# Kernel tuning notes

Measured on AMD Instinct MI355X. Metric: run time of the kernel, lower is better.

## Reference

```python
import jax, jax.numpy as jnp
import numpy as np

NUM_HEADS = 1
SR = 8
DIM = 64
EPS = 1e-5


def _layernorm(x, g, b):
    mu = jnp.mean(x, axis=-1, keepdims=True)
    var = jnp.mean(jnp.square(x - mu), axis=-1, keepdims=True)
    return (x - mu) * jax.lax.rsqrt(var + EPS) * g + b


def _sr_pool(x, h, w, s):
    # x: [B, N, C] with N = h*w -> avg-pool spatially by s -> [B, (h//s)*(w//s), C]
    B, N, C = x.shape
    xi = x.transpose(0, 2, 1).reshape(B, C, h, w)
    xi = xi.reshape(B, C, h // s, s, w // s, s).mean(axis=(3, 5))
    return xi.reshape(B, C, -1).transpose(0, 2, 1)


def _branch(q, x_src, h, w, kv_w, norm_g, norm_b, proj_w, proj_b, scale):
    B, N, C = x_src.shape
    hd = C // NUM_HEADS
    xp = _layernorm(_sr_pool(x_src, h, w, SR), norm_g, norm_b)  # [B, Nk, C]
    kv = (xp @ kv_w.T).reshape(B, -1, 2, NUM_HEADS, hd).transpose(2, 0, 3, 1, 4)
    k, v = kv[0], kv[1]  # [B, H, Nk, hd]
    attn = jnp.einsum('bhnd,bhmd->bhnm', q, k) * scale  # [B, H, N, Nk]
    attn = jax.nn.softmax(attn, axis=-1)
    out = jnp.einsum('bhnm,bhmd->bhnd', attn, v)
    out = out.transpose(0, 2, 1, 3).reshape(B, N, C)
    return out @ proj_w.T + proj_b


def setup_inputs() -> dict:
    key = jax.random.key(0)
    ks = jax.random.split(key, 10)
    B, h, w, C = 4, 128, 128, DIM
    N = h * w
    sd = 1.0 / np.sqrt(C)
    return {
        'x1': jax.random.normal(ks[0], (B, N, C), jnp.float32),
        'x2': jax.random.normal(ks[1], (B, N, C), jnp.float32),
        'h': h,
        'w': w,
        'q1_w': jax.random.uniform(ks[2], (C, C), jnp.float32, -sd, sd),
        'kv1_w': jax.random.uniform(ks[3], (2 * C, C), jnp.float32, -sd, sd),
        'kv2_w': jax.random.uniform(ks[4], (2 * C, C), jnp.float32, -sd, sd),
        'norm1_g': jnp.ones((C,), jnp.float32),
        'norm1_b': jnp.zeros((C,), jnp.float32),
        'norm2_g': jnp.ones((C,), jnp.float32),
        'norm2_b': jnp.zeros((C,), jnp.float32),
        'proj1_w': jax.random.uniform(ks[5], (C, C), jnp.float32, -sd, sd),
        'proj1_b': jnp.zeros((C,), jnp.float32),
        'proj2_w': jax.random.uniform(ks[6], (C, C), jnp.float32, -sd, sd),
        'proj2_b': jnp.zeros((C,), jnp.float32),
    }


def reference(x1, x2, h, w, q1_w, kv1_w, kv2_w, norm1_g, norm1_b,
              norm2_g, norm2_b, proj1_w, proj1_b, proj2_w, proj2_b):
    B, N, C = x1.shape
    hd = C // NUM_HEADS
    scale = hd ** -0.5
    # NOTE: original code uses self.q1 for BOTH q1 and q2 (bug-faithful).
    q1 = (x1 @ q1_w.T).reshape(B, N, NUM_HEADS, hd).transpose(0, 2, 1, 3)
    q2 = (x2 @ q1_w.T).reshape(B, N, NUM_HEADS, hd).transpose(0, 2, 1, 3)
    o1 = _branch(q1, x1, h, w, kv1_w, norm1_g, norm1_b, proj1_w, proj1_b, scale)
    o2 = _branch(q2, x2, h, w, kv2_w, norm2_g, norm2_b, proj2_w, proj2_b, scale)
    return (o1, o2)
```

## Files before the change

### kernel.cpp

```cpp
#include <hip/hip_runtime.h>
#include <math.h>

#define CH 64
#define SRV 8
#define HV 128
#define WV 128
#define NTOK (HV*WV)
#define NKV 256
#define POOLW 16
#define KVIMG 65536

typedef __attribute__((ext_vector_type(8))) short bf16x8;
typedef __attribute__((ext_vector_type(16))) float f32x16;

__device__ __forceinline__ unsigned short f2bf(float x) {
    unsigned u = __float_as_uint(x);
    return (unsigned short)((u + 0x7fffu + ((u >> 16) & 1u)) >> 16);
}
__device__ __forceinline__ unsigned pkbf(float a, float b) {
    return (unsigned)f2bf(a) | ((unsigned)f2bf(b) << 16);
}
__device__ __forceinline__ void swap32(unsigned a, unsigned b, unsigned &oa, unsigned &ob) {
    unsigned ax = (unsigned)__shfl_xor((int)a, 32);
    unsigned bx = (unsigned)__shfl_xor((int)b, 32);
    const bool lo = (threadIdx.x & 32) == 0;
    oa = lo ? a : bx;
    ob = lo ? ax : b;
}

__global__ __launch_bounds__(64) void fused_pool_ln_kv(
    const float* __restrict__ x1, const float* __restrict__ x2,
    const float* __restrict__ kv1w, const float* __restrict__ kv2w,
    const float* __restrict__ n1g, const float* __restrict__ n1b,
    const float* __restrict__ n2g, const float* __restrict__ n2b,
    const float* __restrict__ q1w,
    const float* __restrict__ p1w, const float* __restrict__ p2w,
    char* __restrict__ kvbuf, int B)
{
    const int c = threadIdx.x;
    const int blk = blockIdx.x;
    const int m = blk % NKV;
    const int t = blk / NKV;
    const int b = t % B;
    const int branch = t / B;

    const float* x   = branch ? x2   : x1;
    const float* kvw = branch ? kv2w : kv1w;
    const float* g   = branch ? n2g  : n1g;
    const float* be  = branch ? n2b  : n1b;
    const float* pw  = branch ? p2w  : p1w;

    const int ph = m / POOLW, pwc = m % POOLW;
    const float* xb = x + ((size_t)b * NTOK) * CH;

    float sum = 0.f;
    for (int dy = 0; dy < SRV; ++dy) {
        const int y = ph * SRV + dy;
        const float* xr = xb + ((size_t)(y * WV + pwc * SRV)) * CH + c;
        #pragma unroll
        for (int dx = 0; dx < SRV; ++dx)
            sum += xr[dx * CH];
    }
    float v = sum * (1.f / 64.f);

    float mu = v;
    #pragma unroll
    for (int o = 32; o; o >>= 1) mu += __shfl_xor(mu, o);
    mu *= (1.f / 64.f);
    float d = v - mu;
    float var = d * d;
    #pragma unroll
    for (int o = 32; o; o >>= 1) var += __shfl_xor(var, o);
    var *= (1.f / 64.f);
    float xp = d * rsqrtf(var + 1e-5f) * g[c] + be[c];

    __shared__ float sx[CH];
    __shared__ float kb[CH];
    __shared__ float vb[CH];
    sx[c] = xp;
    __syncthreads();

    float ka = 0.f, va = 0.f;
    #pragma unroll
    for (int dd = 0; dd < CH; ++dd) {
        const float xd = sx[dd];
        ka += xd * kvw[(size_t)c * CH + dd];
        va += xd * kvw[(size_t)(CH + c) * CH + dd];
    }
    kb[c] = ka;
    vb[c] = va;
    __syncthreads();

    float k2 = 0.f, v2 = 0.f;
    #pragma unroll
    for (int j = 0; j < CH; ++j) {
        k2 += kb[j] * q1w[(size_t)j * CH + c];
        v2 += vb[j] * pw[(size_t)c * CH + j];
    }
    k2 *= 0.125f;

    char* base = kvbuf + (size_t)(branch * B + b) * KVIMG;
    *(unsigned short*)(base + m * 128 + ((2 * c) ^ ((m & 7) << 4))) = f2bf(k2);
    *(unsigned short*)(base + 32768 + c * 512 + ((2 * m) ^ ((c & 7) << 4))) = f2bf(v2);
}

__global__ __launch_bounds__(256, 2) void fused_attn_mfma(
    const float* __restrict__ x1, const float* __restrict__ x2,
    const char* __restrict__ kvbuf,
    const float* __restrict__ p1b, const float* __restrict__ p2b,
    float* __restrict__ out, int B)
{
    extern __shared__ char KV[];
    const int tiles = NTOK / 128;
    const int blk = blockIdx.x;
    const int branch = blk / (B * tiles);
    const int rem = blk - branch * (B * tiles);
    const int b = rem / tiles;
    const int tile = rem - b * tiles;
    const int rowbase = tile * 128;

    const float* x  = branch ? x2  : x1;
    const float* pb = branch ? p2b : p1b;
    const char* kvbase = kvbuf + (size_t)(branch * B + b) * KVIMG;

    {
        const int4* src = (const int4*)kvbase;
        int4* dst = (int4*)KV;
        #pragma unroll
        for (int i = 0; i < 16; ++i)
            dst[i * 256 + threadIdx.x] = src[i * 256 + threadIdx.x];
    }
    __syncthreads();

    const int tid = threadIdx.x;
    const int lane = tid & 63;
    const int wv = tid >> 6;
    const int l31 = lane & 31;
    const int hi = lane >> 5;
    const int hi16 = hi * 16, hi8 = hi * 8;
    const int row = rowbase + wv * 32 + l31;
    const float* xr = x + ((size_t)b * NTOK + row) * CH;

    union U8 { bf16x8 v; unsigned d[4]; };

    bf16x8 xf[4];
    #pragma unroll
    for (int kc = 0; kc < 4; ++kc) {
        const float* xp = xr + kc * 16 + hi8;
        const float4 a  = *(const float4*)xp;
        const float4 c4 = *(const float4*)(xp + 4);
        U8 u;
        u.d[0] = pkbf(a.x, a.y);  u.d[1] = pkbf(a.z, a.w);
        u.d[2] = pkbf(c4.x, c4.y); u.d[3] = pkbf(c4.z, c4.w);
        xf[kc] = u.v;
    }

    f32x16 acc[8];
    #pragma unroll
    for (int kb8 = 0; kb8 < 8; ++kb8)
        #pragma unroll
        for (int r = 0; r < 16; ++r) acc[kb8][r] = 0.f;

    #pragma unroll
    for (int kc = 0; kc < 4; ++kc) {
        #pragma unroll
        for (int kb8 = 0; kb8 < 8; ++kb8) {
            const int key = kb8 * 32 + l31;
            const int off = key * 128 + ((kc * 32 + hi16) ^ ((key & 7) << 4));
            const bf16x8 kf = *(const bf16x8*)(KV + off);
            acc[kb8] = __builtin_amdgcn_mfma_f32_32x32x16_bf16(kf, xf[kc], acc[kb8], 0, 0, 0);
        }
    }

    float lsum = 0.f;
    bf16x8 pvB[16];
    #pragma unroll
    for (int kb8 = 0; kb8 < 8; ++kb8) {
        float p[16];
        #pragma unroll
        for (int r = 0; r < 16; ++r) { p[r] = __expf(acc[kb8][r]); lsum += p[r]; }
        unsigned q0, q1, q2, q3;
        U8 u;
        swap32(pkbf(p[0], p[1]),  pkbf(p[4], p[5]),  q0, q2);
        swap32(pkbf(p[2], p[3]),  pkbf(p[6], p[7]),  q1, q3);
        u.d[0] = q0; u.d[1] = q1; u.d[2] = q2; u.d[3] = q3;
        pvB[2 * kb8] = u.v;
        swap32(pkbf(p[8], p[9]),   pkbf(p[12], p[13]), q0, q2);
        swap32(pkbf(p[10], p[11]), pkbf(p[14], p[15]), q1, q3);
        u.d[0] = q0; u.d[1] = q1; u.d[2] = q2; u.d[3] = q3;
        pvB[2 * kb8 + 1] = u.v;
    }
    const float lfull = lsum + __shfl_xor(lsum, 32);
    const float invl = 1.f / lfull;

    f32x16 oac[2];
    #pragma unroll
    for (int df = 0; df < 2; ++df)
        #pragma unroll
        for (int r = 0; r < 16; ++r) oac[df][r] = 0.f;

    #pragma unroll
    for (int t = 0; t < 16; ++t) {
        #pragma unroll
        for (int df = 0; df < 2; ++df) {
            const int d = df * 32 + l31;
            const int off = 32768 + d * 512 + ((t * 32 + hi16) ^ ((d & 7) << 4));
            const bf16x8 vf = *(const bf16x8*)(KV + off);
            oac[df] = __builtin_amdgcn_mfma_f32_32x32x16_bf16(vf, pvB[t], oac[df], 0, 0, 0);
        }
    }

    float* orow = out + ((size_t)(branch * B + b) * NTOK + row) * CH;
    #pragma unroll
    for (int df = 0; df < 2; ++df) {
        #pragma unroll
        for (int q = 0; q < 4; ++q) {
            const int d0 = df * 32 + q * 8 + hi * 4;
            const float4 bias = *(const float4*)(pb + d0);
            float4 w;
            w.x = oac[df][4 * q + 0] * invl + bias.x;
            w.y = oac[df][4 * q + 1] * invl + bias.y;
            w.z = oac[df][4 * q + 2] * invl + bias.z;
            w.w = oac[df][4 * q + 3] * invl + bias.w;
            *(float4*)(orow + d0) = w;
        }
    }
}

extern "C" void kernel_launch(void* const* d_in, const int* in_sizes, int n_in,
                              void* d_out, int out_size, void* d_ws, size_t ws_size,
                              hipStream_t stream) {
    const float* x1   = (const float*)d_in[0];
    const float* x2   = (const float*)d_in[1];
    const float* q1w  = (const float*)d_in[4];
    const float* kv1w = (const float*)d_in[5];
    const float* kv2w = (const float*)d_in[6];
    const float* n1g  = (const float*)d_in[7];
    const float* n1b  = (const float*)d_in[8];
    const float* n2g  = (const float*)d_in[9];
    const float* n2b  = (const float*)d_in[10];
    const float* p1w  = (const float*)d_in[11];
    const float* p1b  = (const float*)d_in[12];
    const float* p2w  = (const float*)d_in[13];
    const float* p2b  = (const float*)d_in[14];

    const int B = in_sizes[0] / (NTOK * CH);
    char* kvbuf = (char*)d_ws;

    fused_pool_ln_kv<<<2 * B * NKV, 64, 0, stream>>>(
        x1, x2, kv1w, kv2w, n1g, n1b, n2g, n2b, q1w, p1w, p2w, kvbuf, B);

    fused_attn_mfma<<<2 * B * (NTOK / 128), 256, KVIMG, stream>>>(
        x1, x2, kvbuf, p1b, p2b, (float*)d_out, B);
}
```

Measured before the change: 46.23 us.

## Process two row tiles per block with async KV LDS loads and prefetch

```diff
diff --git a/kernel.cpp b/kernel.cpp
--- a/kernel.cpp
+++ b/kernel.cpp
@@ -9,6 +9,7 @@
 #define NKV 256
 #define POOLW 16
 #define KVIMG 65536
+#define NITER 2
 
 typedef __attribute__((ext_vector_type(8))) short bf16x8;
 typedef __attribute__((ext_vector_type(16))) float f32x16;
@@ -17,18 +18,34 @@
     unsigned u = __float_as_uint(x);
     return (unsigned short)((u + 0x7fffu + ((u >> 16) & 1u)) >> 16);
 }
-__device__ __forceinline__ unsigned pkbf(float a, float b) {
-    return (unsigned)f2bf(a) | ((unsigned)f2bf(b) << 16);
-}
-__device__ __forceinline__ void swap32(unsigned a, unsigned b, unsigned &oa, unsigned &ob) {
+
+__device__ __forceinline__ unsigned cvt_pk(float lo, float hi) {
+    unsigned r;
+    asm("v_cvt_pk_bf16_f32 %0, %1, %2" : "=v"(r) : "v"(lo), "v"(hi));
+    return r;
+}
+
+__device__ __forceinline__ void plswap(unsigned a, unsigned b,
+                                       unsigned &oa, unsigned &ob) {
+#if __has_builtin(__builtin_amdgcn_permlane32_swap)
+    auto r = __builtin_amdgcn_permlane32_swap(a, b, false, false);
+    oa = r[0]; ob = r[1];
+#else
     unsigned ax = (unsigned)__shfl_xor((int)a, 32);
     unsigned bx = (unsigned)__shfl_xor((int)b, 32);
     const bool lo = (threadIdx.x & 32) == 0;
     oa = lo ? a : bx;
     ob = lo ? ax : b;
-}
-
-__global__ __launch_bounds__(64) void fused_pool_ln_kv(
+#endif
+}
+
+__device__ __forceinline__ void gload_lds16(const void* g, void* l) {
+    __builtin_amdgcn_global_load_lds(
+        (const __attribute__((address_space(1))) void*)g,
+        (__attribute__((address_space(3))) void*)l, 16, 0, 0);
+}
+
+__global__ __launch_bounds__(256) void fused_pool_ln_kv(
     const float* __restrict__ x1, const float* __restrict__ x2,
     const float* __restrict__ kv1w, const float* __restrict__ kv2w,
     const float* __restrict__ n1g, const float* __restrict__ n1b,
@@ -37,16 +54,17 @@
     const float* __restrict__ p1w, const float* __restrict__ p2w,
     char* __restrict__ kvbuf, int B)
 {
-    const int c = threadIdx.x;
-    const int blk = blockIdx.x;
-    const int m = blk % NKV;
-    const int t = blk / NKV;
+    const int c  = threadIdx.x & 63;
+    const int wv = threadIdx.x >> 6;
+    const int g  = blockIdx.x * 4 + wv;
+    const int m = g % NKV;
+    const int t = g / NKV;
     const int b = t % B;
     const int branch = t / B;
 
     const float* x   = branch ? x2   : x1;
     const float* kvw = branch ? kv2w : kv1w;
-    const float* g   = branch ? n2g  : n1g;
+    const float* gg  = branch ? n2g  : n1g;
     const float* be  = branch ? n2b  : n1b;
     const float* pw  = branch ? p2w  : p1w;
 
@@ -72,30 +90,30 @@
     #pragma unroll
     for (int o = 32; o; o >>= 1) var += __shfl_xor(var, o);
     var *= (1.f / 64.f);
-    float xp = d * rsqrtf(var + 1e-5f) * g[c] + be[c];
-
-    __shared__ float sx[CH];
-    __shared__ float kb[CH];
-    __shared__ float vb[CH];
-    sx[c] = xp;
+    float xp = d * rsqrtf(var + 1e-5f) * gg[c] + be[c];
+
+    __shared__ float sx[4][CH];
+    __shared__ float kb[4][CH];
+    __shared__ float vb[4][CH];
+    sx[wv][c] = xp;
     __syncthreads();
 
     float ka = 0.f, va = 0.f;
     #pragma unroll
     for (int dd = 0; dd < CH; ++dd) {
-        const float xd = sx[dd];
+        const float xd = sx[wv][dd];
         ka += xd * kvw[(size_t)c * CH + dd];
         va += xd * kvw[(size_t)(CH + c) * CH + dd];
     }
-    kb[c] = ka;
-    vb[c] = va;
+    kb[wv][c] = ka;
+    vb[wv][c] = va;
     __syncthreads();
 
     float k2 = 0.f, v2 = 0.f;
     #pragma unroll
     for (int j = 0; j < CH; ++j) {
-        k2 += kb[j] * q1w[(size_t)j * CH + c];
-        v2 += vb[j] * pw[(size_t)c * CH + j];
+        k2 += kb[wv][j] * q1w[(size_t)j * CH + c];
+        v2 += vb[wv][j] * pw[(size_t)c * CH + j];
     }
     k2 *= 0.125f;
 
@@ -111,26 +129,16 @@
     float* __restrict__ out, int B)
 {
     extern __shared__ char KV[];
-    const int tiles = NTOK / 128;
+    const int tpg = NTOK / (128 * NITER);
     const int blk = blockIdx.x;
-    const int branch = blk / (B * tiles);
-    const int rem = blk - branch * (B * tiles);
-    const int b = rem / tiles;
-    const int tile = rem - b * tiles;
-    const int rowbase = tile * 128;
+    const int branch = blk / (B * tpg);
+    const int rem = blk - branch * (B * tpg);
+    const int b = rem / tpg;
+    const int tg = rem - b * tpg;
 
     const float* x  = branch ? x2  : x1;
     const float* pb = branch ? p2b : p1b;
     const char* kvbase = kvbuf + (size_t)(branch * B + b) * KVIMG;
-
-    {
-        const int4* src = (const int4*)kvbase;
-        int4* dst = (int4*)KV;
-        #pragma unroll
-        for (int i = 0; i < 16; ++i)
-            dst[i * 256 + threadIdx.x] = src[i * 256 + threadIdx.x];
-    }
-    __syncthreads();
 
     const int tid = threadIdx.x;
     const int lane = tid & 63;
@@ -138,91 +146,126 @@
     const int l31 = lane & 31;
     const int hi = lane >> 5;
     const int hi16 = hi * 16, hi8 = hi * 8;
-    const int row = rowbase + wv * 32 + l31;
-    const float* xr = x + ((size_t)b * NTOK + row) * CH;
+    const int swz = (l31 & 7) << 4;
+
+    {
+        #pragma unroll
+        for (int i = 0; i < 16; ++i)
+            gload_lds16(kvbase + i * 4096 + wv * 1024 + (lane << 4),
+                        KV + i * 4096 + wv * 1024);
+    }
+
+    const int rowb0 = tg * (128 * NITER) + wv * 32 + l31;
+    float4 xq[8];
+    {
+        const float* xr = x + ((size_t)b * NTOK + rowb0) * CH;
+        #pragma unroll
+        for (int kc = 0; kc < 4; ++kc) {
+            xq[2 * kc]     = *(const float4*)(xr + kc * 16 + hi8);
+            xq[2 * kc + 1] = *(const float4*)(xr + kc * 16 + hi8 + 4);
+        }
+    }
+    __syncthreads();
 
     union U8 { bf16x8 v; unsigned d[4]; };
 
-    bf16x8 xf[4];
-    #pragma unroll
-    for (int kc = 0; kc < 4; ++kc) {
-        const float* xp = xr + kc * 16 + hi8;
-        const float4 a  = *(const float4*)xp;
-        const float4 c4 = *(const float4*)(xp + 4);
-        U8 u;
-        u.d[0] = pkbf(a.x, a.y);  u.d[1] = pkbf(a.z, a.w);
-        u.d[2] = pkbf(c4.x, c4.y); u.d[3] = pkbf(c4.z, c4.w);
-        xf[kc] = u.v;
-    }
-
-    f32x16 acc[8];
-    #pragma unroll
-    for (int kb8 = 0; kb8 < 8; ++kb8)
-        #pragma unroll
-        for (int r = 0; r < 16; ++r) acc[kb8][r] = 0.f;
-
-    #pragma unroll
-    for (int kc = 0; kc < 4; ++kc) {
-        #pragma unroll
-        for (int kb8 = 0; kb8 < 8; ++kb8) {
-            const int key = kb8 * 32 + l31;
-            const int off = key * 128 + ((kc * 32 + hi16) ^ ((key & 7) << 4));
-            const bf16x8 kf = *(const bf16x8*)(KV + off);
-            acc[kb8] = __builtin_amdgcn_mfma_f32_32x32x16_bf16(kf, xf[kc], acc[kb8], 0, 0, 0);
-        }
-    }
-
-    float lsum = 0.f;
-    bf16x8 pvB[16];
-    #pragma unroll
-    for (int kb8 = 0; kb8 < 8; ++kb8) {
-        float p[16];
-        #pragma unroll
-        for (int r = 0; r < 16; ++r) { p[r] = __expf(acc[kb8][r]); lsum += p[r]; }
-        unsigned q0, q1, q2, q3;
-        U8 u;
-        swap32(pkbf(p[0], p[1]),  pkbf(p[4], p[5]),  q0, q2);
-        swap32(pkbf(p[2], p[3]),  pkbf(p[6], p[7]),  q1, q3);
-        u.d[0] = q0; u.d[1] = q1; u.d[2] = q2; u.d[3] = q3;
-        pvB[2 * kb8] = u.v;
-        swap32(pkbf(p[8], p[9]),   pkbf(p[12], p[13]), q0, q2);
-        swap32(pkbf(p[10], p[11]), pkbf(p[14], p[15]), q1, q3);
-        u.d[0] = q0; u.d[1] = q1; u.d[2] = q2; u.d[3] = q3;
-        pvB[2 * kb8 + 1] = u.v;
-    }
-    const float lfull = lsum + __shfl_xor(lsum, 32);
-    const float invl = 1.f / lfull;
-
-    f32x16 oac[2];
-    #pragma unroll
-    for (int df = 0; df < 2; ++df)
-        #pragma unroll
-        for (int r = 0; r < 16; ++r) oac[df][r] = 0.f;
-
-    #pragma unroll
-    for (int t = 0; t < 16; ++t) {
+    #pragma unroll
+    for (int it = 0; it < NITER; ++it) {
+        const int row = rowb0 + it * 128;
+
+        bf16x8 xf[4];
+        #pragma unroll
+        for (int kc = 0; kc < 4; ++kc) {
+            const float4 a  = xq[2 * kc];
+            const float4 c4 = xq[2 * kc + 1];
+            U8 u;
+            u.d[0] = cvt_pk(a.x, a.y);   u.d[1] = cvt_pk(a.z, a.w);
+            u.d[2] = cvt_pk(c4.x, c4.y); u.d[3] = cvt_pk(c4.z, c4.w);
+            xf[kc] = u.v;
+        }
+        if (it + 1 < NITER) {
+            const float* xr = x + ((size_t)b * NTOK + row + 128) * CH;
+            #pragma unroll
+            for (int kc = 0; kc < 4; ++kc) {
+                xq[2 * kc]     = *(const float4*)(xr + kc * 16 + hi8);
+                xq[2 * kc + 1] = *(const float4*)(xr + kc * 16 + hi8 + 4);
+            }
+        }
+
+        float lsum0 = 0.f, lsum1 = 0.f;
+        bf16x8 pvB[16];
+        #pragma unroll
+        for (int kp = 0; kp < 4; ++kp) {
+            f32x16 a0, a1;
+            #pragma unroll
+            for (int r = 0; r < 16; ++r) { a0[r] = 0.f; a1[r] = 0.f; }
+            const int key0 = kp * 64 + l31;
+            __builtin_amdgcn_s_setprio(1);
+            #pragma unroll
+            for (int kc = 0; kc < 4; ++kc) {
+                const int co = (kc * 32 + hi16) ^ swz;
+                const bf16x8 k0 = *(const bf16x8*)(KV + key0 * 128 + co);
+                const bf16x8 k1 = *(const bf16x8*)(KV + (key0 + 32) * 128 + co);
+                a0 = __builtin_amdgcn_mfma_f32_32x32x16_bf16(k0, xf[kc], a0, 0, 0, 0);
+                a1 = __builtin_amdgcn_mfma_f32_32x32x16_bf16(k1, xf[kc], a1, 0, 0, 0);
+            }
+            __builtin_amdgcn_s_setprio(0);
+            float p0[16], p1[16];
+            #pragma unroll
+            for (int r = 0; r < 16; ++r) {
+                p0[r] = __expf(a0[r]); lsum0 += p0[r];
+                p1[r] = __expf(a1[r]); lsum1 += p1[r];
+            }
+            #pragma unroll
+            for (int h = 0; h < 2; ++h) {
+                const float* p = h ? p1 : p0;
+                unsigned q0, q1, q2, q3;
+                U8 u;
+                plswap(cvt_pk(p[0], p[1]), cvt_pk(p[4], p[5]), q0, q2);
+                plswap(cvt_pk(p[2], p[3]), cvt_pk(p[6], p[7]), q1, q3);
+                u.d[0] = q0; u.d[1] = q1; u.d[2] = q2; u.d[3] = q3;
+                pvB[4 * kp + 2 * h] = u.v;
+                plswap(cvt_pk(p[8], p[9]),   cvt_pk(p[12], p[13]), q0, q2);
+                plswap(cvt_pk(p[10], p[11]), cvt_pk(p[14], p[15]), q1, q3);
+                u.d[0] = q0; u.d[1] = q1; u.d[2] = q2; u.d[3] = q3;
+                pvB[4 * kp + 2 * h + 1] = u.v;
+            }
+        }
+        float lsum = lsum0 + lsum1;
+        const float lfull = lsum + __shfl_xor(lsum, 32);
+        const float invl = 1.f / lfull;
+
+        f32x16 oac[2];
+        #pragma unroll
+        for (int df = 0; df < 2; ++df)
+            #pragma unroll
+            for (int r = 0; r < 16; ++r) oac[df][r] = 0.f;
+
+        __builtin_amdgcn_s_setprio(1);
+        #pragma unroll
+        for (int t = 0; t < 16; ++t) {
+            const int co = (t * 32 + hi16) ^ swz;
+            const bf16x8 vf0 = *(const bf16x8*)(KV + 32768 + l31 * 512 + co);
+            const bf16x8 vf1 = *(const bf16x8*)(KV + 32768 + (32 + l31) * 512 + co);
+            oac[0] = __builtin_amdgcn_mfma_f32_32x32x16_bf16(vf0, pvB[t], oac[0], 0, 0, 0);
+            oac[1] = __builtin_amdgcn_mfma_f32_32x32x16_bf16(vf1, pvB[t], oac[1], 0, 0, 0);
+        }
+        __builtin_amdgcn_s_setprio(0);
+
+        float* orow = out + ((size_t)(branch * B + b) * NTOK + row) * CH;
         #pragma unroll
         for (int df = 0; df < 2; ++df) {
-            const int d = df * 32 + l31;
-            const int off = 32768 + d * 512 + ((t * 32 + hi16) ^ ((d & 7) << 4));
-            const bf16x8 vf = *(const bf16x8*)(KV + off);
-            oac[df] = __builtin_amdgcn_mfma_f32_32x32x16_bf16(vf, pvB[t], oac[df], 0, 0, 0);
-        }
-    }
-
-    float* orow = out + ((size_t)(branch * B + b) * NTOK + row) * CH;
-    #pragma unroll
-    for (int df = 0; df < 2; ++df) {
-        #pragma unroll
-        for (int q = 0; q < 4; ++q) {
-            const int d0 = df * 32 + q * 8 + hi * 4;
-            const float4 bias = *(const float4*)(pb + d0);
-            float4 w;
-            w.x = oac[df][4 * q + 0] * invl + bias.x;
-            w.y = oac[df][4 * q + 1] * invl + bias.y;
-            w.z = oac[df][4 * q + 2] * invl + bias.z;
-            w.w = oac[df][4 * q + 3] * invl + bias.w;
-            *(float4*)(orow + d0) = w;
+            #pragma unroll
+            for (int q = 0; q < 4; ++q) {
+                const int d0 = df * 32 + q * 8 + hi * 4;
+                const float4 bias = *(const float4*)(pb + d0);
+                float4 w;
+                w.x = oac[df][4 * q + 0] * invl + bias.x;
+                w.y = oac[df][4 * q + 1] * invl + bias.y;
+                w.z = oac[df][4 * q + 2] * invl + bias.z;
+                w.w = oac[df][4 * q + 3] * invl + bias.w;
+                *(float4*)(orow + d0) = w;
+            }
         }
     }
 }
@@ -247,9 +290,9 @@
     const int B = in_sizes[0] / (NTOK * CH);
     char* kvbuf = (char*)d_ws;
 
-    fused_pool_ln_kv<<<2 * B * NKV, 64, 0, stream>>>(
+    fused_pool_ln_kv<<<2 * B * NKV / 4, 256, 0, stream>>>(
         x1, x2, kv1w, kv2w, n1g, n1b, n2g, n2b, q1w, p1w, p2w, kvbuf, B);
 
-    fused_attn_mfma<<<2 * B * (NTOK / 128), 256, KVIMG, stream>>>(
+    fused_attn_mfma<<<2 * B * (NTOK / (128 * NITER)), 256, KVIMG, stream>>>(
         x1, x2, kvbuf, p1b, p2b, (float*)d_out, B);
 }
```

New measurement: 41.37 us. -10.5%, faster.
